# Kernel optimization log

Hardware: AMD Instinct MI355X
Metric: run time of the kernel (lower is better)

Reference implementation:

```python
import jax, jax.numpy as jnp
import numpy as np

NUM_NODES = 50000
NUM_RELS = 256
D = 256            # node_in_feat
TEXT_D = 256       # text_emb_dim
T_TOTAL = 24       # number of unique timestep graphs
E = 20000          # edges per timestep graph
B = 16             # batch of query times
SEQ_LEN = 7


def setup_inputs() -> dict:
    key = jax.random.key(0)
    ks = jax.random.split(key, 12)
    s = 1.0 / np.sqrt(D)
    return {
        "node_embeds": jax.random.normal(ks[0], (NUM_NODES, D), jnp.float32),
        "text_emb": jax.random.normal(ks[1], (T_TOTAL, E, TEXT_D), jnp.float32),
        "text_w_W": jax.random.uniform(ks[2], (TEXT_D, D), jnp.float32, -s, s),
        "text_w_b": jax.random.uniform(ks[3], (D,), jnp.float32, -s, s),
        "edge_w_W": jax.random.uniform(ks[4], (3 * D, D), jnp.float32, -s, s),
        "edge_w_b": jax.random.uniform(ks[5], (D,), jnp.float32, -s, s),
        "gru_Wih": jax.random.uniform(ks[6], (D, 3 * D), jnp.float32, -s, s),
        "gru_Whh": jax.random.uniform(ks[7], (D, 3 * D), jnp.float32, -s, s),
        "gru_bih": jax.random.uniform(ks[8], (3 * D,), jnp.float32, -s, s),
        "gru_bhh": jax.random.uniform(ks[9], (3 * D,), jnp.float32, -s, s),
        "edge_src": jax.random.randint(ks[10], (T_TOTAL, E), 0, NUM_NODES, jnp.int32),
        "edge_dst": jax.random.randint(jax.random.fold_in(ks[10], 1), (T_TOTAL, E), 0, NUM_NODES, jnp.int32),
        "edge_rel": jax.random.randint(jax.random.fold_in(ks[10], 2), (T_TOTAL, E), 0, NUM_RELS, jnp.int32),
        "time_idx": jax.random.randint(ks[11], (B, SEQ_LEN), 0, T_TOTAL, jnp.int32),
    }


def _gru(seqs, Wih, Whh, bih, bhh):
    # seqs: [B, R, S, d] -> run GRU over S, return final hidden [B, R, d]
    xs = jnp.moveaxis(seqs, 2, 0)  # [S, B, R, d]
    h0 = jnp.zeros(seqs.shape[:2] + (seqs.shape[-1],), seqs.dtype)

    def step(h, x):
        gi = x @ Wih + bih            # [B, R, 3d]
        gh = h @ Whh + bhh
        i_r, i_z, i_n = jnp.split(gi, 3, axis=-1)
        h_r, h_z, h_n = jnp.split(gh, 3, axis=-1)
        r = jax.nn.sigmoid(i_r + h_r)
        z = jax.nn.sigmoid(i_z + h_z)
        n = jnp.tanh(i_n + r * h_n)
        h_new = (1.0 - z) * n + z * h
        return h_new, None

    h_final, _ = jax.lax.scan(step, h0, xs)
    return h_final


def reference(node_embeds, text_emb, text_w_W, text_w_b, edge_w_W, edge_w_b,
              gru_Wih, gru_Whh, gru_bih, gru_bhh,
              edge_src, edge_dst, edge_rel, time_idx):
    # edge text projection (text_w): [T, E, D]
    text_h = text_emb @ text_w_W + text_w_b
    # gather node embeddings per edge endpoint
    h_src = node_embeds[edge_src]  # [T, E, D]
    h_dst = node_embeds[edge_dst]  # [T, E, D]
    # concat + edge MLP + ReLU: e_h = relu(edge_w([src || text || dst]))
    e = jnp.concatenate([h_src, text_h, h_dst], axis=-1)  # [T, E, 3D]
    e_h = jax.nn.relu(e @ edge_w_W + edge_w_b)            # [T, E, D]

    # scatter-mean of edge embeddings by relation type per timestep graph;
    # relations absent in a graph get zeros (init_rel_embeds = zeros)
    seg = lambda v, r: jax.ops.segment_sum(v, r, num_segments=NUM_RELS)
    sums = jax.vmap(seg)(e_h, edge_rel)                               # [T, R, D]
    counts = jax.vmap(seg)(jnp.ones(edge_rel.shape, e_h.dtype), edge_rel)  # [T, R]
    counts = counts[..., None]
    rel_emb = jnp.where(counts > 0, sums / jnp.maximum(counts, 1.0), 0.0)  # [T, R, D]

    # per query time: gather its window of timestep rel-embeddings and run
    # the GRU over time (relations act as the GRU batch dim, like transpose(0,1))
    seqs = rel_emb[time_idx]                 # [B, S, R, D]
    seqs = jnp.swapaxes(seqs, 1, 2)          # [B, R, S, D]
    hn = _gru(seqs, gru_Wih, gru_Whh, gru_bih, gru_bhh)  # [B, R, D]
    return hn
```

## Files before the change

kernel.cpp:

```cpp
#include <hip/hip_runtime.h>
#include <cstdint>
#include <cstddef>

#define NNODES 50000
#define NPAD   50048
#define NRELS  256
#define DIM    256
#define TT     24
#define EE     20000
#define BATCH  16
#define SEQQ   7

typedef __bf16 bf16;
typedef __bf16 bf16x8 __attribute__((ext_vector_type(8)));
typedef float  f32x4  __attribute__((ext_vector_type(4)));

__device__ __forceinline__ void gload16(const void* g, void* l){
  __builtin_amdgcn_global_load_lds((const __attribute__((address_space(1))) void*)g,
                                   (__attribute__((address_space(3))) void*)l, 16, 0, 0);
}


__global__ void k_cvt8(const float* __restrict__ in, bf16* __restrict__ out, int n8){
  int i = blockIdx.x*256 + threadIdx.x;
  if (i >= n8) return;
  const float4* p = (const float4*)in + (size_t)i*2;
  float4 a = p[0], b = p[1];
  bf16x8 o;
  o[0]=(bf16)a.x; o[1]=(bf16)a.y; o[2]=(bf16)a.z; o[3]=(bf16)a.w;
  o[4]=(bf16)b.x; o[5]=(bf16)b.y; o[6]=(bf16)b.z; o[7]=(bf16)b.w;
  ((bf16x8*)out)[i] = o;
}

__global__ void k_build_wbt(const float* __restrict__ tW, const float* __restrict__ eW,
                            bf16* __restrict__ WbT){
  int n = blockIdx.x, j = threadIdx.x;
  WbT[(size_t)n*768 + j]       = (bf16)eW[(size_t)j*256 + n];
  WbT[(size_t)n*768 + 512 + j] = (bf16)eW[(size_t)(512+j)*256 + n];
  float acc = 0.f;
  for (int m=0; m<256; ++m) acc += tW[(size_t)j*256 + m] * eW[(size_t)(256+m)*256 + n];
  WbT[(size_t)n*768 + 256 + j] = (bf16)acc;
}

__global__ void k_bias(const float* __restrict__ tb, const float* __restrict__ eW,
                       const float* __restrict__ eb, float* __restrict__ bf){
  int n = threadIdx.x;
  float acc = eb[n];
  for (int m=0; m<256; ++m) acc += tb[m] * eW[(size_t)(256+m)*256 + n];
  bf[n] = acc;
}

__global__ void k_gruWT(const float* __restrict__ W, bf16* __restrict__ WT){
  int n = blockIdx.x, k = threadIdx.x;
  WT[(size_t)n*256 + k] = (bf16)W[(size_t)k*768 + n];
}

__global__ void k_hist(const int* __restrict__ rel, int* __restrict__ counts,
                       int* __restrict__ offs, int* __restrict__ cursor){
  __shared__ int hist[256];
  __shared__ int scan[256];
  int t = blockIdx.x, tid = threadIdx.x;
  hist[tid] = 0;
  __syncthreads();
  for (int e = tid; e < EE; e += 256) atomicAdd(&hist[rel[(size_t)t*EE + e]], 1);
  __syncthreads();
  int v = hist[tid];
  scan[tid] = v;
  __syncthreads();
  for (int d=1; d<256; d<<=1){
    int add = (tid >= d) ? scan[tid-d] : 0;
    __syncthreads();
    scan[tid] += add;
    __syncthreads();
  }
  int ex = scan[tid] - v;
  counts[t*256+tid] = v;
  offs[t*256+tid]   = ex;
  cursor[t*256+tid] = ex;
}

__global__ void k_perm(const int* __restrict__ rel, const int* __restrict__ esrc,
                       const int* __restrict__ edst, int* __restrict__ cursor,
                       int* __restrict__ perm, int* __restrict__ src_p,
                       int* __restrict__ dst_p){
  int t = blockIdx.y;
  int e = blockIdx.x*256 + threadIdx.x;
  if (e < EE){
    int r = rel[(size_t)t*EE + e];
    int p = atomicAdd(&cursor[t*256 + r], 1);
    perm[(size_t)t*EE + p]  = e;
    src_p[(size_t)t*EE + p] = esrc[(size_t)t*EE + e];
    dst_p[(size_t)t*EE + p] = edst[(size_t)t*EE + e];
  }
}

template<int TEXTMODE>
__global__ __launch_bounds__(256) void k_proj(
    const bf16* __restrict__ Abf, const float* __restrict__ Afp,
    const int* __restrict__ perm, const bf16* __restrict__ WbT, int koff,
    const float* __restrict__ bias, bf16* __restrict__ out)
{
  int m0 = blockIdx.x*128;
  int tid = threadIdx.x, lane = tid&63, w = tid>>6;
  int l15 = lane&15, lq = lane>>4;
  int c0 = w*64;
  __shared__ __align__(16) bf16 Al[128*32];
  __shared__ __align__(16) bf16 Bl[256*32];

  int r0 = tid>>2, r1 = 64 + (tid>>2);
  int part = tid&3;
  int pp0 = part ^ ((r0>>1)&3);
  const float* aP0 = nullptr; const float* aP1 = nullptr;
  if (TEXTMODE){
    size_t g0 = (size_t)m0 + r0;  int t0 = (int)(g0/EE);
    size_t g1 = (size_t)m0 + r1;  int t1 = (int)(g1/EE);
    aP0 = Afp + ((size_t)t0*EE + perm[g0])*256;
    aP1 = Afp + ((size_t)t1*EE + perm[g1])*256;
  }
  float bias4[4];
  if (TEXTMODE){
    #pragma unroll
    for (int ni=0;ni<4;++ni) bias4[ni] = bias[c0 + ni*16 + l15];
  }

  f32x4 acc[8][4];
  f32x4 z4 = {0.f,0.f,0.f,0.f};
  #pragma unroll
  for (int mi=0;mi<8;++mi)
    #pragma unroll
    for (int ni=0;ni<4;++ni) acc[mi][ni]=z4;

  for (int ks=0; ks<8; ++ks){
    int k0 = ks*32;
    if (TEXTMODE){
      {
        const float* sp = aP0 + k0 + pp0*8;
        float4 u = ((const float4*)sp)[0], v = ((const float4*)sp)[1];
        bf16x8 o;
        o[0]=(bf16)u.x; o[1]=(bf16)u.y; o[2]=(bf16)u.z; o[3]=(bf16)u.w;
        o[4]=(bf16)v.x; o[5]=(bf16)v.y; o[6]=(bf16)v.z; o[7]=(bf16)v.w;
        *(bf16x8*)((char*)Al + (size_t)tid*16) = o;
      }
      {
        const float* sp = aP1 + k0 + pp0*8;
        float4 u = ((const float4*)sp)[0], v = ((const float4*)sp)[1];
        bf16x8 o;
        o[0]=(bf16)u.x; o[1]=(bf16)u.y; o[2]=(bf16)u.z; o[3]=(bf16)u.w;
        o[4]=(bf16)v.x; o[5]=(bf16)v.y; o[6]=(bf16)v.z; o[7]=(bf16)v.w;
        *(bf16x8*)((char*)Al + (size_t)(256+tid)*16) = o;
      }
    } else {
      #pragma unroll
      for (int p=0;p<2;++p){
        int c = p*256 + tid;
        int rw = c>>2, prt = c&3;
        int pp = prt ^ ((rw>>1)&3);
        const char* src = (const char*)(Abf + (size_t)(m0+rw)*256 + k0) + pp*16;
        gload16(src, (char*)Al + (size_t)(p*256 + w*64)*16);
      }
    }
    #pragma unroll
    for (int p=0;p<4;++p){
      int c = p*256 + tid;
      int nn = c>>2, prt = c&3;
      int pp = prt ^ ((nn>>1)&3);
      const char* src = (const char*)(WbT + (size_t)nn*768 + koff + k0) + pp*16;
      gload16(src, (char*)Bl + (size_t)(p*256 + w*64)*16);
    }
    __syncthreads();
    bf16x8 a[8], b[4];
    #pragma unroll
    for (int ni=0;ni<4;++ni){
      int nn = c0 + ni*16 + l15;
      b[ni] = *(const bf16x8*)((const char*)Bl + (size_t)nn*64 + (size_t)((lq ^ ((nn>>1)&3))*16));
    }
    #pragma unroll
    for (int mi=0;mi<8;++mi){
      int rw = mi*16 + l15;
      a[mi] = *(const bf16x8*)((const char*)Al + (size_t)rw*64 + (size_t)((lq ^ ((rw>>1)&3))*16));
    }
    #pragma unroll
    for (int mi=0;mi<8;++mi)
      #pragma unroll
      for (int ni=0;ni<4;++ni)
        acc[mi][ni] = __builtin_amdgcn_mfma_f32_16x16x32_bf16(a[mi], b[ni], acc[mi][ni], 0,0,0);
    __syncthreads();
  }
  #pragma unroll
  for (int ni=0;ni<4;++ni){
    int col = c0 + ni*16 + l15;
    #pragma unroll
    for (int mi=0;mi<8;++mi){
      #pragma unroll
      for (int q=0;q<4;++q){
        int row = m0 + mi*16 + lq*4 + q;
        float v = acc[mi][ni][q];
        if (TEXTMODE) v += bias4[ni];
        out[(size_t)row*256 + col] = (bf16)v;
      }
    }
  }
}

__global__ __launch_bounds__(256) void k_comb(
    const bf16* __restrict__ P, const bf16* __restrict__ Q,
    const bf16* __restrict__ T, const int* __restrict__ src_p,
    const int* __restrict__ dst_p, const int* __restrict__ counts,
    const int* __restrict__ offs, bf16* __restrict__ rel_bf)
{
  int r = blockIdx.x, t = blockIdx.y;
  int tid = threadIdx.x;
  int tr = t*256 + r;
  int nE = counts[tr];
  if (nE == 0){
    rel_bf[(size_t)tr*256 + tid] = (bf16)0.f;
    return;
  }
  int base = offs[tr];
  int es = tid>>5, cg = (tid&31)*8;
  float acc[8];
  #pragma unroll
  for (int j=0;j<8;++j) acc[j]=0.f;
  for (int i = es; i < nE; i += 8){
    size_t g = (size_t)t*EE + base + i;
    int s = src_p[g], d = dst_p[g];
    bf16x8 pv = *(const bf16x8*)(P + (size_t)s*256 + cg);
    bf16x8 qv = *(const bf16x8*)(Q + (size_t)d*256 + cg);
    bf16x8 tv = *(const bf16x8*)(T + g*256 + cg);
    #pragma unroll
    for (int j=0;j<8;++j)
      acc[j] += fmaxf((float)pv[j] + (float)qv[j] + (float)tv[j], 0.f);
  }
  __shared__ float red[8][256];
  #pragma unroll
  for (int j=0;j<8;++j) red[es][cg+j] = acc[j];
  __syncthreads();
  float s = 0.f;
  #pragma unroll
  for (int e=0;e<8;++e) s += red[e][tid];
  rel_bf[(size_t)tr*256 + tid] = (bf16)(s / (float)nE);
}

__global__ __launch_bounds__(256) void k_gemm(
    const bf16* __restrict__ A, const bf16* __restrict__ BT,
    const float* __restrict__ bias, float* __restrict__ Out)
{
  int m0 = blockIdx.x*128, n0 = blockIdx.y*128;
  int tid = threadIdx.x, lane = tid&63, w = tid>>6;
  int l15 = lane&15, lq = lane>>4;
  __shared__ __align__(16) bf16 Al[128*32];
  __shared__ __align__(16) bf16 Bl[128*32];
  int wr = (w&1)*64, wc = (w>>1)*64;
  f32x4 acc[4][4];
  f32x4 z4 = {0.f,0.f,0.f,0.f};
  #pragma unroll
  for (int mi=0;mi<4;++mi)
    #pragma unroll
    for (int ni=0;ni<4;++ni) acc[mi][ni]=z4;
  for (int ks=0; ks<8; ++ks){
    int k0 = ks*32;
    #pragma unroll
    for (int p=0;p<2;++p){
      int c = p*256 + tid;
      int rw = c>>2, part = c&3;
      int pp = part ^ ((rw>>1)&3);
      const char* src = (const char*)(A + (size_t)(m0+rw)*256 + k0) + pp*16;
      gload16(src, (char*)Al + (size_t)(p*256 + w*64)*16);
    }
    #pragma unroll
    for (int p=0;p<2;++p){
      int c = p*256 + tid;
      int nn = c>>2, part = c&3;
      int pp = part ^ ((nn>>1)&3);
      const char* src = (const char*)(BT + (size_t)(n0+nn)*256 + k0) + pp*16;
      gload16(src, (char*)Bl + (size_t)(p*256 + w*64)*16);
    }
    __syncthreads();
    bf16x8 a[4], b[4];
    #pragma unroll
    for (int mi=0;mi<4;++mi){
      int rw = wr + mi*16 + l15;
      a[mi] = *(const bf16x8*)((const char*)Al + (size_t)rw*64 + (size_t)((lq ^ ((rw>>1)&3))*16));
    }
    #pragma unroll
    for (int ni=0;ni<4;++ni){
      int nn = wc + ni*16 + l15;
      b[ni] = *(const bf16x8*)((const char*)Bl + (size_t)nn*64 + (size_t)((lq ^ ((nn>>1)&3))*16));
    }
    #pragma unroll
    for (int mi=0;mi<4;++mi)
      #pragma unroll
      for (int ni=0;ni<4;++ni)
        acc[mi][ni] = __builtin_amdgcn_mfma_f32_16x16x32_bf16(a[mi], b[ni], acc[mi][ni], 0,0,0);
    __syncthreads();
  }
  #pragma unroll
  for (int ni=0;ni<4;++ni){
    int col = n0 + wc + ni*16 + l15;
    float bv = bias[col];
    #pragma unroll
    for (int mi=0;mi<4;++mi){
      #pragma unroll
      for (int q=0;q<4;++q){
        int row = m0 + wr + mi*16 + lq*4 + q;
        Out[(size_t)row*768 + col] = acc[mi][ni][q] + bv;
      }
    }
  }
}

__global__ void k_update(const float* __restrict__ GI, const float* __restrict__ gh,
                         const float* __restrict__ bhh, const int* __restrict__ time_idx,
                         const float* __restrict__ h_in, float* __restrict__ h_out,
                         bf16* __restrict__ hbf_out, float* __restrict__ out_final, int s)
{
  int row = blockIdx.x;
  int d = threadIdx.x;
  int b = row >> 8, rr = row & 255;
  int t = time_idx[b*SEQQ + s];
  size_t gib = (size_t)(t*256 + rr)*768;
  float ir = GI[gib + d], iz = GI[gib + 256 + d], inn = GI[gib + 512 + d];
  float hr, hz, hn;
  if (s == 0){ hr = bhh[d]; hz = bhh[256+d]; hn = bhh[512+d]; }
  else { size_t gb = (size_t)row*768; hr = gh[gb+d]; hz = gh[gb+256+d]; hn = gh[gb+512+d]; }
  float rg = 1.f/(1.f + __expf(-(ir+hr)));
  float zz = 1.f/(1.f + __expf(-(iz+hz)));
  float nn = tanhf(inn + rg*hn);
  float hp = (s==0) ? 0.f : h_in[(size_t)row*256 + d];
  float hv = (1.f - zz)*nn + zz*hp;
  if (s == SEQQ-1){
    out_final[(size_t)row*256 + d] = hv;
  } else {
    h_out[(size_t)row*256 + d] = hv;
    hbf_out[(size_t)row*256 + d] = (bf16)hv;
  }
}

extern "C" void kernel_launch(void* const* d_in, const int* in_sizes, int n_in,
                              void* d_out, int out_size, void* d_ws, size_t ws_size,
                              hipStream_t stream)
{
  (void)in_sizes; (void)n_in; (void)out_size; (void)ws_size;
  const float* node_embeds = (const float*)d_in[0];
  const float* text_emb    = (const float*)d_in[1];
  const float* text_w_W    = (const float*)d_in[2];
  const float* text_w_b    = (const float*)d_in[3];
  const float* edge_w_W    = (const float*)d_in[4];
  const float* edge_w_b    = (const float*)d_in[5];
  const float* gru_Wih     = (const float*)d_in[6];
  const float* gru_Whh     = (const float*)d_in[7];
  const float* gru_bih     = (const float*)d_in[8];
  const float* gru_bhh     = (const float*)d_in[9];
  const int* edge_src      = (const int*)d_in[10];
  const int* edge_dst      = (const int*)d_in[11];
  const int* edge_rel      = (const int*)d_in[12];
  const int* time_idx      = (const int*)d_in[13];
  float* out = (float*)d_out;
  char* ws = (char*)d_ws;

  size_t o = 0;
  bf16*  WbT    = (bf16*) (ws + o); o += (size_t)768*256*2;
  bf16*  WihT   = (bf16*) (ws + o); o += (size_t)768*256*2;
  bf16*  WhhT   = (bf16*) (ws + o); o += (size_t)768*256*2;
  float* bfused = (float*)(ws + o); o += 1024;
  bf16*  node_bf= (bf16*) (ws + o); o += (size_t)NPAD*256*2;
  int*   counts = (int*)  (ws + o); o += (size_t)TT*256*4;
  int*   offs   = (int*)  (ws + o); o += (size_t)TT*256*4;
  int*   cursor = (int*)  (ws + o); o += (size_t)TT*256*4;
  int*   perm   = (int*)  (ws + o); o += (size_t)TT*EE*4;
  int*   src_p  = (int*)  (ws + o); o += (size_t)TT*EE*4;
  int*   dst_p  = (int*)  (ws + o); o += (size_t)TT*EE*4;
  bf16*  rel_bf = (bf16*) (ws + o); o += (size_t)TT*256*256*2;
  bf16*  P      = (bf16*) (ws + o); o += (size_t)NPAD*256*2;
  bf16*  Q      = (bf16*) (ws + o); o += (size_t)NPAD*256*2;
  size_t oT = o;
  bf16*  Tproj  = (bf16*) (ws + oT);
  float* GI     = (float*)(ws + oT); size_t o2 = oT + (size_t)TT*256*768*4;
  float* h      = (float*)(ws + o2); o2 += (size_t)4096*256*4;
  bf16*  hbf    = (bf16*) (ws + o2); o2 += (size_t)4096*256*2;
  float* gh     = (float*)(ws + o2); o2 += (size_t)4096*768*4;

  k_cvt8<<<6250,256,0,stream>>>(node_embeds, node_bf, NNODES*256/8);
  k_build_wbt<<<256,256,0,stream>>>(text_w_W, edge_w_W, WbT);
  k_bias<<<1,256,0,stream>>>(text_w_b, edge_w_W, edge_w_b, bfused);
  k_gruWT<<<768,256,0,stream>>>(gru_Wih, WihT);
  k_gruWT<<<768,256,0,stream>>>(gru_Whh, WhhT);
  k_hist<<<TT,256,0,stream>>>(edge_rel, counts, offs, cursor);
  k_perm<<<dim3((EE+255)/256,TT),256,0,stream>>>(edge_rel, edge_src, edge_dst,
                                                 cursor, perm, src_p, dst_p);
  k_proj<0><<<NPAD/128,256,0,stream>>>(node_bf, nullptr, nullptr, WbT, 0,   nullptr, P);
  k_proj<0><<<NPAD/128,256,0,stream>>>(node_bf, nullptr, nullptr, WbT, 512, nullptr, Q);
  k_proj<1><<<TT*EE/128,256,0,stream>>>(nullptr, text_emb, perm, WbT, 256, bfused, Tproj);
  k_comb<<<dim3(256,TT),256,0,stream>>>(P, Q, Tproj, src_p, dst_p, counts, offs, rel_bf);
  k_gemm<<<dim3(48,6),256,0,stream>>>(rel_bf, WihT, gru_bih, GI);
  for (int s=0; s<SEQQ; ++s){
    if (s > 0)
      k_gemm<<<dim3(32,6),256,0,stream>>>(hbf, WhhT, gru_bhh, gh);
    k_update<<<4096,256,0,stream>>>(GI, gh, gru_bhh, time_idx, h, h, hbf, out, s);
  }
}
```

Baseline: 671.1 us.

## Fuse text projection with edge combine and segmented atomic scatter-mean

The text-embedding GEMM is merged with the edge MLP epilogue: each tile adds the gathered P/Q node projections plus bias, applies ReLU in registers, and reduces rows sharing a (time, relation) run before doing atomicAdd into an fp32 rel_sum buffer. A small mean kernel then divides by counts. This removes writing and re-reading the bf16 Tproj intermediate and the separate k_comb gather pass. The cost is a memset, serial run detection by one thread per block, and float atomics that make the summation order nondeterministic. The MFMA operand order is also swapped so outputs can be stored as bf16x4 vectors.

```diff
diff --git a/kernel.cpp b/kernel.cpp
--- a/kernel.cpp
+++ b/kernel.cpp
@@ -12,6 +12,7 @@
 #define SEQQ   7
 
 typedef __bf16 bf16;
+typedef __bf16 bf16x4 __attribute__((ext_vector_type(4)));
 typedef __bf16 bf16x8 __attribute__((ext_vector_type(8)));
 typedef float  f32x4  __attribute__((ext_vector_type(4)));
 
@@ -81,24 +82,24 @@
 
 __global__ void k_perm(const int* __restrict__ rel, const int* __restrict__ esrc,
                        const int* __restrict__ edst, int* __restrict__ cursor,
-                       int* __restrict__ perm, int* __restrict__ src_p,
-                       int* __restrict__ dst_p){
+                       int* __restrict__ gperm, int* __restrict__ src_p,
+                       int* __restrict__ dst_p, int* __restrict__ tr_p){
   int t = blockIdx.y;
   int e = blockIdx.x*256 + threadIdx.x;
   if (e < EE){
     int r = rel[(size_t)t*EE + e];
     int p = atomicAdd(&cursor[t*256 + r], 1);
-    perm[(size_t)t*EE + p]  = e;
-    src_p[(size_t)t*EE + p] = esrc[(size_t)t*EE + e];
-    dst_p[(size_t)t*EE + p] = edst[(size_t)t*EE + e];
-  }
-}
-
-template<int TEXTMODE>
-__global__ __launch_bounds__(256) void k_proj(
-    const bf16* __restrict__ Abf, const float* __restrict__ Afp,
-    const int* __restrict__ perm, const bf16* __restrict__ WbT, int koff,
-    const float* __restrict__ bias, bf16* __restrict__ out)
+    size_t g = (size_t)t*EE + p;
+    gperm[g] = t*EE + e;
+    src_p[g] = esrc[(size_t)t*EE + e];
+    dst_p[g] = edst[(size_t)t*EE + e];
+    tr_p[g]  = t*256 + r;
+  }
+}
+
+__global__ __launch_bounds__(256) void k_projn(
+    const bf16* __restrict__ Abf, const bf16* __restrict__ WbT, int koff,
+    bf16* __restrict__ out)
 {
   int m0 = blockIdx.x*128;
   int tid = threadIdx.x, lane = tid&63, w = tid>>6;
@@ -107,22 +108,6 @@
   __shared__ __align__(16) bf16 Al[128*32];
   __shared__ __align__(16) bf16 Bl[256*32];
 
-  int r0 = tid>>2, r1 = 64 + (tid>>2);
-  int part = tid&3;
-  int pp0 = part ^ ((r0>>1)&3);
-  const float* aP0 = nullptr; const float* aP1 = nullptr;
-  if (TEXTMODE){
-    size_t g0 = (size_t)m0 + r0;  int t0 = (int)(g0/EE);
-    size_t g1 = (size_t)m0 + r1;  int t1 = (int)(g1/EE);
-    aP0 = Afp + ((size_t)t0*EE + perm[g0])*256;
-    aP1 = Afp + ((size_t)t1*EE + perm[g1])*256;
-  }
-  float bias4[4];
-  if (TEXTMODE){
-    #pragma unroll
-    for (int ni=0;ni<4;++ni) bias4[ni] = bias[c0 + ni*16 + l15];
-  }
-
   f32x4 acc[8][4];
   f32x4 z4 = {0.f,0.f,0.f,0.f};
   #pragma unroll
@@ -132,32 +117,13 @@
 
   for (int ks=0; ks<8; ++ks){
     int k0 = ks*32;
-    if (TEXTMODE){
-      {
-        const float* sp = aP0 + k0 + pp0*8;
-        float4 u = ((const float4*)sp)[0], v = ((const float4*)sp)[1];
-        bf16x8 o;
-        o[0]=(bf16)u.x; o[1]=(bf16)u.y; o[2]=(bf16)u.z; o[3]=(bf16)u.w;
-        o[4]=(bf16)v.x; o[5]=(bf16)v.y; o[6]=(bf16)v.z; o[7]=(bf16)v.w;
-        *(bf16x8*)((char*)Al + (size_t)tid*16) = o;
-      }
-      {
-        const float* sp = aP1 + k0 + pp0*8;
-        float4 u = ((const float4*)sp)[0], v = ((const float4*)sp)[1];
-        bf16x8 o;
-        o[0]=(bf16)u.x; o[1]=(bf16)u.y; o[2]=(bf16)u.z; o[3]=(bf16)u.w;
-        o[4]=(bf16)v.x; o[5]=(bf16)v.y; o[6]=(bf16)v.z; o[7]=(bf16)v.w;
-        *(bf16x8*)((char*)Al + (size_t)(256+tid)*16) = o;
-      }
-    } else {
-      #pragma unroll
-      for (int p=0;p<2;++p){
-        int c = p*256 + tid;
-        int rw = c>>2, prt = c&3;
-        int pp = prt ^ ((rw>>1)&3);
-        const char* src = (const char*)(Abf + (size_t)(m0+rw)*256 + k0) + pp*16;
-        gload16(src, (char*)Al + (size_t)(p*256 + w*64)*16);
-      }
+    #pragma unroll
+    for (int p=0;p<2;++p){
+      int c = p*256 + tid;
+      int rw = c>>2, prt = c&3;
+      int pp = prt ^ ((rw>>1)&3);
+      const char* src = (const char*)(Abf + (size_t)(m0+rw)*256 + k0) + pp*16;
+      gload16(src, (char*)Al + (size_t)(p*256 + w*64)*16);
     }
     #pragma unroll
     for (int p=0;p<4;++p){
@@ -168,7 +134,7 @@
       gload16(src, (char*)Bl + (size_t)(p*256 + w*64)*16);
     }
     __syncthreads();
-    bf16x8 a[8], b[4];
+    bf16x8 b[4];
     #pragma unroll
     for (int ni=0;ni<4;++ni){
       int nn = c0 + ni*16 + l15;
@@ -177,68 +143,169 @@
     #pragma unroll
     for (int mi=0;mi<8;++mi){
       int rw = mi*16 + l15;
-      a[mi] = *(const bf16x8*)((const char*)Al + (size_t)rw*64 + (size_t)((lq ^ ((rw>>1)&3))*16));
-    }
-    #pragma unroll
-    for (int mi=0;mi<8;++mi)
+      bf16x8 a = *(const bf16x8*)((const char*)Al + (size_t)rw*64 + (size_t)((lq ^ ((rw>>1)&3))*16));
       #pragma unroll
       for (int ni=0;ni<4;++ni)
-        acc[mi][ni] = __builtin_amdgcn_mfma_f32_16x16x32_bf16(a[mi], b[ni], acc[mi][ni], 0,0,0);
-    __syncthreads();
-  }
-  #pragma unroll
-  for (int ni=0;ni<4;++ni){
-    int col = c0 + ni*16 + l15;
+        acc[mi][ni] = __builtin_amdgcn_mfma_f32_16x16x32_bf16(b[ni], a, acc[mi][ni], 0,0,0);
+    }
+    __syncthreads();
+  }
+  #pragma unroll
+  for (int mi=0;mi<8;++mi){
+    int row = m0 + mi*16 + l15;
+    #pragma unroll
+    for (int ni=0;ni<4;++ni){
+      bf16x4 o;
+      #pragma unroll
+      for (int q=0;q<4;++q) o[q] = (bf16)acc[mi][ni][q];
+      *(bf16x4*)(out + (size_t)row*256 + c0 + ni*16 + lq*4) = o;
+    }
+  }
+}
+
+__global__ __launch_bounds__(256) void k_tcomb(
+    const float* __restrict__ text, const int* __restrict__ gperm,
+    const bf16* __restrict__ WbT, const float* __restrict__ bfused,
+    const bf16* __restrict__ P, const bf16* __restrict__ Q,
+    const int* __restrict__ src_p, const int* __restrict__ dst_p,
+    const int* __restrict__ tr_p, float* __restrict__ rel_sum)
+{
+  int m0 = blockIdx.x*128;
+  int tid = threadIdx.x, lane = tid&63, w = tid>>6;
+  int l15 = lane&15, lq = lane>>4;
+  int c0 = w*64;
+  __shared__ __align__(16) bf16 Al[128*32];
+  __shared__ __align__(16) bf16 Bl[256*32];
+  __shared__ int trA[128], sI[128], dI[128];
+  __shared__ int runS[129], runT[128], nRunS;
+
+  if (tid < 128){
+    int g = m0 + tid;
+    trA[tid] = tr_p[g];
+    sI[tid]  = src_p[g];
+    dI[tid]  = dst_p[g];
+  }
+  __syncthreads();
+  if (tid == 0){
+    int nR = 0;
+    for (int i=0;i<128;++i){
+      if (i==0 || trA[i]!=trA[i-1]){ runS[nR]=i; runT[nR]=trA[i]; ++nR; }
+    }
+    runS[nR] = 128;
+    nRunS = nR;
+  }
+
+  int r0 = tid>>2;
+  int part = tid&3;
+  int pp0 = part ^ ((r0>>1)&3);
+  const float* aP0 = text + (size_t)gperm[m0 + r0]*256;
+  const float* aP1 = text + (size_t)gperm[m0 + 64 + r0]*256;
+
+  f32x4 acc[8][4];
+  f32x4 z4 = {0.f,0.f,0.f,0.f};
+  #pragma unroll
+  for (int mi=0;mi<8;++mi)
+    #pragma unroll
+    for (int ni=0;ni<4;++ni) acc[mi][ni]=z4;
+
+  for (int ks=0; ks<8; ++ks){
+    int k0 = ks*32;
+    {
+      const float* sp = aP0 + k0 + pp0*8;
+      float4 u = ((const float4*)sp)[0], v = ((const float4*)sp)[1];
+      bf16x8 o;
+      o[0]=(bf16)u.x; o[1]=(bf16)u.y; o[2]=(bf16)u.z; o[3]=(bf16)u.w;
+      o[4]=(bf16)v.x; o[5]=(bf16)v.y; o[6]=(bf16)v.z; o[7]=(bf16)v.w;
+      *(bf16x8*)((char*)Al + (size_t)tid*16) = o;
+      sp = aP1 + k0 + pp0*8;
+      u = ((const float4*)sp)[0]; v = ((const float4*)sp)[1];
+      o[0]=(bf16)u.x; o[1]=(bf16)u.y; o[2]=(bf16)u.z; o[3]=(bf16)u.w;
+      o[4]=(bf16)v.x; o[5]=(bf16)v.y; o[6]=(bf16)v.z; o[7]=(bf16)v.w;
+      *(bf16x8*)((char*)Al + (size_t)(256+tid)*16) = o;
+    }
+    #pragma unroll
+    for (int p=0;p<4;++p){
+      int c = p*256 + tid;
+      int nn = c>>2, prt = c&3;
+      int pp = prt ^ ((nn>>1)&3);
+      const char* src = (const char*)(WbT + (size_t)nn*768 + 256 + k0) + pp*16;
+      gload16(src, (char*)Bl + (size_t)(p*256 + w*64)*16);
+    }
+    __syncthreads();
+    bf16x8 b[4];
+    #pragma unroll
+    for (int ni=0;ni<4;++ni){
+      int nn = c0 + ni*16 + l15;
+      b[ni] = *(const bf16x8*)((const char*)Bl + (size_t)nn*64 + (size_t)((lq ^ ((nn>>1)&3))*16));
+    }
     #pragma unroll
     for (int mi=0;mi<8;++mi){
+      int rw = mi*16 + l15;
+      bf16x8 a = *(const bf16x8*)((const char*)Al + (size_t)rw*64 + (size_t)((lq ^ ((rw>>1)&3))*16));
+      #pragma unroll
+      for (int ni=0;ni<4;++ni)
+        acc[mi][ni] = __builtin_amdgcn_mfma_f32_16x16x32_bf16(b[ni], a, acc[mi][ni], 0,0,0);
+    }
+    __syncthreads();
+  }
+
+  float4 bias4[4];
+  #pragma unroll
+  for (int ni=0;ni<4;++ni)
+    bias4[ni] = *(const float4*)(bfused + c0 + ni*16 + lq*4);
+
+  #pragma unroll
+  for (int mi=0;mi<8;++mi){
+    int row = mi*16 + l15;
+    int srow = sI[row], drow = dI[row];
+    #pragma unroll
+    for (int ni=0;ni<4;++ni){
+      bf16x4 pv = *(const bf16x4*)(P + (size_t)srow*256 + c0 + ni*16 + lq*4);
+      bf16x4 qv = *(const bf16x4*)(Q + (size_t)drow*256 + c0 + ni*16 + lq*4);
+      f32x4 t4 = acc[mi][ni];
+      t4[0] = fmaxf(t4[0] + (float)pv[0] + (float)qv[0] + bias4[ni].x, 0.f);
+      t4[1] = fmaxf(t4[1] + (float)pv[1] + (float)qv[1] + bias4[ni].y, 0.f);
+      t4[2] = fmaxf(t4[2] + (float)pv[2] + (float)qv[2] + bias4[ni].z, 0.f);
+      t4[3] = fmaxf(t4[3] + (float)pv[3] + (float)qv[3] + bias4[ni].w, 0.f);
+      acc[mi][ni] = t4;
+    }
+  }
+
+  int nR = nRunS;
+  for (int k=0; k<nR; ++k){
+    int rs = runS[k], re = runS[k+1], tr = runT[k];
+    float part16[16];
+    #pragma unroll
+    for (int ni=0;ni<4;++ni){
       #pragma unroll
       for (int q=0;q<4;++q){
-        int row = m0 + mi*16 + lq*4 + q;
-        float v = acc[mi][ni][q];
-        if (TEXTMODE) v += bias4[ni];
-        out[(size_t)row*256 + col] = (bf16)v;
+        float s = 0.f;
+        #pragma unroll
+        for (int mi=0;mi<8;++mi){
+          int row = mi*16 + l15;
+          s += (row >= rs && row < re) ? acc[mi][ni][q] : 0.f;
+        }
+        part16[ni*4+q] = s;
       }
     }
-  }
-}
-
-__global__ __launch_bounds__(256) void k_comb(
-    const bf16* __restrict__ P, const bf16* __restrict__ Q,
-    const bf16* __restrict__ T, const int* __restrict__ src_p,
-    const int* __restrict__ dst_p, const int* __restrict__ counts,
-    const int* __restrict__ offs, bf16* __restrict__ rel_bf)
-{
-  int r = blockIdx.x, t = blockIdx.y;
-  int tid = threadIdx.x;
-  int tr = t*256 + r;
-  int nE = counts[tr];
-  if (nE == 0){
-    rel_bf[(size_t)tr*256 + tid] = (bf16)0.f;
-    return;
-  }
-  int base = offs[tr];
-  int es = tid>>5, cg = (tid&31)*8;
-  float acc[8];
-  #pragma unroll
-  for (int j=0;j<8;++j) acc[j]=0.f;
-  for (int i = es; i < nE; i += 8){
-    size_t g = (size_t)t*EE + base + i;
-    int s = src_p[g], d = dst_p[g];
-    bf16x8 pv = *(const bf16x8*)(P + (size_t)s*256 + cg);
-    bf16x8 qv = *(const bf16x8*)(Q + (size_t)d*256 + cg);
-    bf16x8 tv = *(const bf16x8*)(T + g*256 + cg);
-    #pragma unroll
-    for (int j=0;j<8;++j)
-      acc[j] += fmaxf((float)pv[j] + (float)qv[j] + (float)tv[j], 0.f);
-  }
-  __shared__ float red[8][256];
-  #pragma unroll
-  for (int j=0;j<8;++j) red[es][cg+j] = acc[j];
-  __syncthreads();
-  float s = 0.f;
-  #pragma unroll
-  for (int e=0;e<8;++e) s += red[e][tid];
-  rel_bf[(size_t)tr*256 + tid] = (bf16)(s / (float)nE);
+    #pragma unroll
+    for (int m=1; m<16; m<<=1){
+      #pragma unroll
+      for (int s=0;s<16;++s) part16[s] += __shfl_xor(part16[s], m);
+    }
+    float v = part16[0];
+    #pragma unroll
+    for (int s=1;s<16;++s) v = (l15==s) ? part16[s] : v;
+    atomicAdd(&rel_sum[(size_t)tr*256 + c0 + ((l15>>2)<<4) + (lq<<2) + (l15&3)], v);
+  }
+}
+
+__global__ void k_mean(const float* __restrict__ rel_sum, const int* __restrict__ counts,
+                       bf16* __restrict__ rel_bf){
+  int tr = blockIdx.x, c = threadIdx.x;
+  int cnt = counts[tr];
+  float v = (cnt > 0) ? rel_sum[(size_t)tr*256 + c] / (float)cnt : 0.f;
+  rel_bf[(size_t)tr*256 + c] = (bf16)v;
 }
 
 __global__ __launch_bounds__(256) void k_gemm(
@@ -367,18 +434,18 @@
   int*   counts = (int*)  (ws + o); o += (size_t)TT*256*4;
   int*   offs   = (int*)  (ws + o); o += (size_t)TT*256*4;
   int*   cursor = (int*)  (ws + o); o += (size_t)TT*256*4;
-  int*   perm   = (int*)  (ws + o); o += (size_t)TT*EE*4;
+  int*   gperm  = (int*)  (ws + o); o += (size_t)TT*EE*4;
   int*   src_p  = (int*)  (ws + o); o += (size_t)TT*EE*4;
   int*   dst_p  = (int*)  (ws + o); o += (size_t)TT*EE*4;
+  int*   tr_p   = (int*)  (ws + o); o += (size_t)TT*EE*4;
   bf16*  rel_bf = (bf16*) (ws + o); o += (size_t)TT*256*256*2;
   bf16*  P      = (bf16*) (ws + o); o += (size_t)NPAD*256*2;
   bf16*  Q      = (bf16*) (ws + o); o += (size_t)NPAD*256*2;
-  size_t oT = o;
-  bf16*  Tproj  = (bf16*) (ws + oT);
-  float* GI     = (float*)(ws + oT); size_t o2 = oT + (size_t)TT*256*768*4;
-  float* h      = (float*)(ws + o2); o2 += (size_t)4096*256*4;
-  bf16*  hbf    = (bf16*) (ws + o2); o2 += (size_t)4096*256*2;
-  float* gh     = (float*)(ws + o2); o2 += (size_t)4096*768*4;
+  float* rel_sum= (float*)(ws + o); o += (size_t)TT*256*256*4;
+  float* GI     = (float*)(ws + o); o += (size_t)TT*256*768*4;
+  float* h      = (float*)(ws + o); o += (size_t)4096*256*4;
+  bf16*  hbf    = (bf16*) (ws + o); o += (size_t)4096*256*2;
+  float* gh     = (float*)(ws + o); o += (size_t)4096*768*4;
 
   k_cvt8<<<6250,256,0,stream>>>(node_embeds, node_bf, NNODES*256/8);
   k_build_wbt<<<256,256,0,stream>>>(text_w_W, edge_w_W, WbT);
@@ -387,11 +454,13 @@
   k_gruWT<<<768,256,0,stream>>>(gru_Whh, WhhT);
   k_hist<<<TT,256,0,stream>>>(edge_rel, counts, offs, cursor);
   k_perm<<<dim3((EE+255)/256,TT),256,0,stream>>>(edge_rel, edge_src, edge_dst,
-                                                 cursor, perm, src_p, dst_p);
-  k_proj<0><<<NPAD/128,256,0,stream>>>(node_bf, nullptr, nullptr, WbT, 0,   nullptr, P);
-  k_proj<0><<<NPAD/128,256,0,stream>>>(node_bf, nullptr, nullptr, WbT, 512, nullptr, Q);
-  k_proj<1><<<TT*EE/128,256,0,stream>>>(nullptr, text_emb, perm, WbT, 256, bfused, Tproj);
-  k_comb<<<dim3(256,TT),256,0,stream>>>(P, Q, Tproj, src_p, dst_p, counts, offs, rel_bf);
+                                                 cursor, gperm, src_p, dst_p, tr_p);
+  k_projn<<<NPAD/128,256,0,stream>>>(node_bf, WbT, 0,   P);
+  k_projn<<<NPAD/128,256,0,stream>>>(node_bf, WbT, 512, Q);
+  hipMemsetAsync(rel_sum, 0, (size_t)TT*256*256*4, stream);
+  k_tcomb<<<TT*EE/128,256,0,stream>>>(text_emb, gperm, WbT, bfused, P, Q,
+                                      src_p, dst_p, tr_p, rel_sum);
+  k_mean<<<TT*256,256,0,stream>>>(rel_sum, counts, rel_bf);
   k_gemm<<<dim3(48,6),256,0,stream>>>(rel_bf, WihT, gru_bih, GI);
   for (int s=0; s<SEQQ; ++s){
     if (s > 0)
```

Result: slower. 764.4 us (+13.9%).

## Split projection kernel into node and text variants with smaller text tiles

Applied to the files above, without the earlier changes.

The templated projection kernel becomes two kernels. The node one swaps MFMA operand order so each lane can write four contiguous bf16 outputs at once, and it drops the per-row A register array. The text one uses 64-row tiles with launch_bounds(256,4) for higher occupancy and precomputes global permutation indices in k_perm to avoid a per-row division. The fused bias add moves from the text projection output into k_comb's accumulation loop, which adds a little per-edge arithmetic there.

```diff
diff --git a/kernel.cpp b/kernel.cpp
--- a/kernel.cpp
+++ b/kernel.cpp
@@ -12,6 +12,7 @@
 #define SEQQ   7
 
 typedef __bf16 bf16;
+typedef __bf16 bf16x4 __attribute__((ext_vector_type(4)));
 typedef __bf16 bf16x8 __attribute__((ext_vector_type(8)));
 typedef float  f32x4  __attribute__((ext_vector_type(4)));
 
@@ -81,24 +82,23 @@
 
 __global__ void k_perm(const int* __restrict__ rel, const int* __restrict__ esrc,
                        const int* __restrict__ edst, int* __restrict__ cursor,
-                       int* __restrict__ perm, int* __restrict__ src_p,
+                       int* __restrict__ gperm, int* __restrict__ src_p,
                        int* __restrict__ dst_p){
   int t = blockIdx.y;
   int e = blockIdx.x*256 + threadIdx.x;
   if (e < EE){
     int r = rel[(size_t)t*EE + e];
     int p = atomicAdd(&cursor[t*256 + r], 1);
-    perm[(size_t)t*EE + p]  = e;
-    src_p[(size_t)t*EE + p] = esrc[(size_t)t*EE + e];
-    dst_p[(size_t)t*EE + p] = edst[(size_t)t*EE + e];
-  }
-}
-
-template<int TEXTMODE>
-__global__ __launch_bounds__(256) void k_proj(
-    const bf16* __restrict__ Abf, const float* __restrict__ Afp,
-    const int* __restrict__ perm, const bf16* __restrict__ WbT, int koff,
-    const float* __restrict__ bias, bf16* __restrict__ out)
+    size_t g = (size_t)t*EE + p;
+    gperm[g] = t*EE + e;
+    src_p[g] = esrc[(size_t)t*EE + e];
+    dst_p[g] = edst[(size_t)t*EE + e];
+  }
+}
+
+__global__ __launch_bounds__(256) void k_projn(
+    const bf16* __restrict__ Abf, const bf16* __restrict__ WbT, int koff,
+    bf16* __restrict__ out)
 {
   int m0 = blockIdx.x*128;
   int tid = threadIdx.x, lane = tid&63, w = tid>>6;
@@ -107,22 +107,6 @@
   __shared__ __align__(16) bf16 Al[128*32];
   __shared__ __align__(16) bf16 Bl[256*32];
 
-  int r0 = tid>>2, r1 = 64 + (tid>>2);
-  int part = tid&3;
-  int pp0 = part ^ ((r0>>1)&3);
-  const float* aP0 = nullptr; const float* aP1 = nullptr;
-  if (TEXTMODE){
-    size_t g0 = (size_t)m0 + r0;  int t0 = (int)(g0/EE);
-    size_t g1 = (size_t)m0 + r1;  int t1 = (int)(g1/EE);
-    aP0 = Afp + ((size_t)t0*EE + perm[g0])*256;
-    aP1 = Afp + ((size_t)t1*EE + perm[g1])*256;
-  }
-  float bias4[4];
-  if (TEXTMODE){
-    #pragma unroll
-    for (int ni=0;ni<4;++ni) bias4[ni] = bias[c0 + ni*16 + l15];
-  }
-
   f32x4 acc[8][4];
   f32x4 z4 = {0.f,0.f,0.f,0.f};
   #pragma unroll
@@ -132,32 +116,13 @@
 
   for (int ks=0; ks<8; ++ks){
     int k0 = ks*32;
-    if (TEXTMODE){
-      {
-        const float* sp = aP0 + k0 + pp0*8;
-        float4 u = ((const float4*)sp)[0], v = ((const float4*)sp)[1];
-        bf16x8 o;
-        o[0]=(bf16)u.x; o[1]=(bf16)u.y; o[2]=(bf16)u.z; o[3]=(bf16)u.w;
-        o[4]=(bf16)v.x; o[5]=(bf16)v.y; o[6]=(bf16)v.z; o[7]=(bf16)v.w;
-        *(bf16x8*)((char*)Al + (size_t)tid*16) = o;
-      }
-      {
-        const float* sp = aP1 + k0 + pp0*8;
-        float4 u = ((const float4*)sp)[0], v = ((const float4*)sp)[1];
-        bf16x8 o;
-        o[0]=(bf16)u.x; o[1]=(bf16)u.y; o[2]=(bf16)u.z; o[3]=(bf16)u.w;
-        o[4]=(bf16)v.x; o[5]=(bf16)v.y; o[6]=(bf16)v.z; o[7]=(bf16)v.w;
-        *(bf16x8*)((char*)Al + (size_t)(256+tid)*16) = o;
-      }
-    } else {
-      #pragma unroll
-      for (int p=0;p<2;++p){
-        int c = p*256 + tid;
-        int rw = c>>2, prt = c&3;
-        int pp = prt ^ ((rw>>1)&3);
-        const char* src = (const char*)(Abf + (size_t)(m0+rw)*256 + k0) + pp*16;
-        gload16(src, (char*)Al + (size_t)(p*256 + w*64)*16);
-      }
+    #pragma unroll
+    for (int p=0;p<2;++p){
+      int c = p*256 + tid;
+      int rw = c>>2, prt = c&3;
+      int pp = prt ^ ((rw>>1)&3);
+      const char* src = (const char*)(Abf + (size_t)(m0+rw)*256 + k0) + pp*16;
+      gload16(src, (char*)Al + (size_t)(p*256 + w*64)*16);
     }
     #pragma unroll
     for (int p=0;p<4;++p){
@@ -168,7 +133,7 @@
       gload16(src, (char*)Bl + (size_t)(p*256 + w*64)*16);
     }
     __syncthreads();
-    bf16x8 a[8], b[4];
+    bf16x8 b[4];
     #pragma unroll
     for (int ni=0;ni<4;++ni){
       int nn = c0 + ni*16 + l15;
@@ -177,36 +142,103 @@
     #pragma unroll
     for (int mi=0;mi<8;++mi){
       int rw = mi*16 + l15;
-      a[mi] = *(const bf16x8*)((const char*)Al + (size_t)rw*64 + (size_t)((lq ^ ((rw>>1)&3))*16));
-    }
-    #pragma unroll
-    for (int mi=0;mi<8;++mi)
+      bf16x8 a = *(const bf16x8*)((const char*)Al + (size_t)rw*64 + (size_t)((lq ^ ((rw>>1)&3))*16));
       #pragma unroll
       for (int ni=0;ni<4;++ni)
-        acc[mi][ni] = __builtin_amdgcn_mfma_f32_16x16x32_bf16(a[mi], b[ni], acc[mi][ni], 0,0,0);
-    __syncthreads();
-  }
-  #pragma unroll
-  for (int ni=0;ni<4;++ni){
-    int col = c0 + ni*16 + l15;
-    #pragma unroll
-    for (int mi=0;mi<8;++mi){
-      #pragma unroll
-      for (int q=0;q<4;++q){
-        int row = m0 + mi*16 + lq*4 + q;
-        float v = acc[mi][ni][q];
-        if (TEXTMODE) v += bias4[ni];
-        out[(size_t)row*256 + col] = (bf16)v;
-      }
+        acc[mi][ni] = __builtin_amdgcn_mfma_f32_16x16x32_bf16(b[ni], a, acc[mi][ni], 0,0,0);
+    }
+    __syncthreads();
+  }
+  #pragma unroll
+  for (int mi=0;mi<8;++mi){
+    int row = m0 + mi*16 + l15;
+    #pragma unroll
+    for (int ni=0;ni<4;++ni){
+      bf16x4 o;
+      #pragma unroll
+      for (int q=0;q<4;++q) o[q] = (bf16)acc[mi][ni][q];
+      *(bf16x4*)(out + (size_t)row*256 + c0 + ni*16 + lq*4) = o;
+    }
+  }
+}
+
+__global__ __launch_bounds__(256,4) void k_projt(
+    const float* __restrict__ text, const int* __restrict__ gperm,
+    const bf16* __restrict__ WbT, bf16* __restrict__ out)
+{
+  int m0 = blockIdx.x*64;
+  int tid = threadIdx.x, lane = tid&63, w = tid>>6;
+  int l15 = lane&15, lq = lane>>4;
+  int c0 = w*64;
+  __shared__ __align__(16) bf16 Al[64*32];
+  __shared__ __align__(16) bf16 Bl[256*32];
+
+  int r0 = tid>>2;
+  int part = tid&3;
+  int pp0 = part ^ ((r0>>1)&3);
+  const float* aP0 = text + (size_t)gperm[m0 + r0]*256;
+
+  f32x4 acc[4][4];
+  f32x4 z4 = {0.f,0.f,0.f,0.f};
+  #pragma unroll
+  for (int mi=0;mi<4;++mi)
+    #pragma unroll
+    for (int ni=0;ni<4;++ni) acc[mi][ni]=z4;
+
+  for (int ks=0; ks<8; ++ks){
+    int k0 = ks*32;
+    {
+      const float* sp = aP0 + k0 + pp0*8;
+      float4 u = ((const float4*)sp)[0], v = ((const float4*)sp)[1];
+      bf16x8 o;
+      o[0]=(bf16)u.x; o[1]=(bf16)u.y; o[2]=(bf16)u.z; o[3]=(bf16)u.w;
+      o[4]=(bf16)v.x; o[5]=(bf16)v.y; o[6]=(bf16)v.z; o[7]=(bf16)v.w;
+      *(bf16x8*)((char*)Al + (size_t)tid*16) = o;
+    }
+    #pragma unroll
+    for (int p=0;p<4;++p){
+      int c = p*256 + tid;
+      int nn = c>>2, prt = c&3;
+      int pp = prt ^ ((nn>>1)&3);
+      const char* src = (const char*)(WbT + (size_t)nn*768 + 256 + k0) + pp*16;
+      gload16(src, (char*)Bl + (size_t)(p*256 + w*64)*16);
+    }
+    __syncthreads();
+    bf16x8 b[4];
+    #pragma unroll
+    for (int ni=0;ni<4;++ni){
+      int nn = c0 + ni*16 + l15;
+      b[ni] = *(const bf16x8*)((const char*)Bl + (size_t)nn*64 + (size_t)((lq ^ ((nn>>1)&3))*16));
+    }
+    #pragma unroll
+    for (int mi=0;mi<4;++mi){
+      int rw = mi*16 + l15;
+      bf16x8 a = *(const bf16x8*)((const char*)Al + (size_t)rw*64 + (size_t)((lq ^ ((rw>>1)&3))*16));
+      #pragma unroll
+      for (int ni=0;ni<4;++ni)
+        acc[mi][ni] = __builtin_amdgcn_mfma_f32_16x16x32_bf16(b[ni], a, acc[mi][ni], 0,0,0);
+    }
+    __syncthreads();
+  }
+  #pragma unroll
+  for (int mi=0;mi<4;++mi){
+    int row = m0 + mi*16 + l15;
+    #pragma unroll
+    for (int ni=0;ni<4;++ni){
+      bf16x4 o;
+      #pragma unroll
+      for (int q=0;q<4;++q) o[q] = (bf16)acc[mi][ni][q];
+      *(bf16x4*)(out + (size_t)row*256 + c0 + ni*16 + lq*4) = o;
     }
   }
 }
 
 __global__ __launch_bounds__(256) void k_comb(
     const bf16* __restrict__ P, const bf16* __restrict__ Q,
-    const bf16* __restrict__ T, const int* __restrict__ src_p,
-    const int* __restrict__ dst_p, const int* __restrict__ counts,
-    const int* __restrict__ offs, bf16* __restrict__ rel_bf)
+    const bf16* __restrict__ T, const float* __restrict__ bfused,
+    const int* __restrict__ src_p, const int* __restrict__ dst_p,
+    const int* __restrict__ counts, const int* __restrict__ offs,
+    bf16* __restrict__ rel_bf)
 {
   int r = blockIdx.x, t = blockIdx.y;
   int tid = threadIdx.x;
@@ -218,6 +250,13 @@
   }
   int base = offs[tr];
   int es = tid>>5, cg = (tid&31)*8;
+  float bb[8];
+  {
+    float4 b0 = *(const float4*)(bfused + cg);
+    float4 b1 = *(const float4*)(bfused + cg + 4);
+    bb[0]=b0.x; bb[1]=b0.y; bb[2]=b0.z; bb[3]=b0.w;
+    bb[4]=b1.x; bb[5]=b1.y; bb[6]=b1.z; bb[7]=b1.w;
+  }
   float acc[8];
   #pragma unroll
   for (int j=0;j<8;++j) acc[j]=0.f;
@@ -229,7 +268,7 @@
     bf16x8 tv = *(const bf16x8*)(T + g*256 + cg);
     #pragma unroll
     for (int j=0;j<8;++j)
-      acc[j] += fmaxf((float)pv[j] + (float)qv[j] + (float)tv[j], 0.f);
+      acc[j] += fmaxf((float)pv[j] + (float)qv[j] + (float)tv[j] + bb[j], 0.f);
   }
   __shared__ float red[8][256];
   #pragma unroll
@@ -367,7 +406,7 @@
   int*   counts = (int*)  (ws + o); o += (size_t)TT*256*4;
   int*   offs   = (int*)  (ws + o); o += (size_t)TT*256*4;
   int*   cursor = (int*)  (ws + o); o += (size_t)TT*256*4;
-  int*   perm   = (int*)  (ws + o); o += (size_t)TT*EE*4;
+  int*   gperm  = (int*)  (ws + o); o += (size_t)TT*EE*4;
   int*   src_p  = (int*)  (ws + o); o += (size_t)TT*EE*4;
   int*   dst_p  = (int*)  (ws + o); o += (size_t)TT*EE*4;
   bf16*  rel_bf = (bf16*) (ws + o); o += (size_t)TT*256*256*2;
@@ -387,11 +426,12 @@
   k_gruWT<<<768,256,0,stream>>>(gru_Whh, WhhT);
   k_hist<<<TT,256,0,stream>>>(edge_rel, counts, offs, cursor);
   k_perm<<<dim3((EE+255)/256,TT),256,0,stream>>>(edge_rel, edge_src, edge_dst,
-                                                 cursor, perm, src_p, dst_p);
-  k_proj<0><<<NPAD/128,256,0,stream>>>(node_bf, nullptr, nullptr, WbT, 0,   nullptr, P);
-  k_proj<0><<<NPAD/128,256,0,stream>>>(node_bf, nullptr, nullptr, WbT, 512, nullptr, Q);
-  k_proj<1><<<TT*EE/128,256,0,stream>>>(nullptr, text_emb, perm, WbT, 256, bfused, Tproj);
-  k_comb<<<dim3(256,TT),256,0,stream>>>(P, Q, Tproj, src_p, dst_p, counts, offs, rel_bf);
+                                                 cursor, gperm, src_p, dst_p);
+  k_projn<<<NPAD/128,256,0,stream>>>(node_bf, WbT, 0,   P);
+  k_projn<<<NPAD/128,256,0,stream>>>(node_bf, WbT, 512, Q);
+  k_projt<<<TT*EE/64,256,0,stream>>>(text_emb, gperm, WbT, Tproj);
+  k_comb<<<dim3(256,TT),256,0,stream>>>(P, Q, Tproj, bfused, src_p, dst_p,
+                                        counts, offs, rel_bf);
   k_gemm<<<dim3(48,6),256,0,stream>>>(rel_bf, WihT, gru_bih, GI);
   for (int s=0; s<SEQQ; ++s){
     if (s > 0)
```

Measured after the change: 636.9 us. 5.1% less time.
